# Kernel optimization log

Hardware: AMD Instinct MI355X
Metric: run time of the kernel (lower is better)

Reference implementation:

```python
import jax, jax.numpy as jnp
import numpy as np

CODE_DIMS = [256, 512, 1024, 2048]
C = 256
BETA = 0.25
B = 64
N = 1024


def setup_inputs() -> dict:
    key = jax.random.key(0)
    ks = jax.random.split(key, 2 + len(CODE_DIMS))
    z_e = jax.random.normal(ks[0], (B, N, C), dtype=jnp.float32)
    expert_idx = jax.random.randint(ks[1], (B,), 0, len(CODE_DIMS))
    s = 1.0 / np.sqrt(C)  # torch uniform init bound
    inp = {"z_e": z_e, "expert_idx": expert_idx}
    for r, K in enumerate(CODE_DIMS):
        inp[f"cb{r}"] = jax.random.uniform(ks[2 + r], (K, C), minval=-s, maxval=s, dtype=jnp.float32)
    return inp


def _vq_expert(z_e, cb):
    # z_e: [B, N, C], cb: [K, C]
    Bz, Nz, Cz = z_e.shape
    zf = z_e.reshape(-1, Cz)                                  # [B*N, C]
    dists = ((zf ** 2).sum(axis=1, keepdims=True)
             + (cb ** 2).sum(axis=1)[None, :]
             - 2.0 * zf @ cb.T)                               # [B*N, K]
    idx = jnp.argmin(dists, axis=1)                           # [B*N]
    z_q = cb[idx].reshape(Bz, Nz, Cz)                         # [B, N, C]
    return z_q, idx.reshape(Bz, Nz)


def reference(z_e, expert_idx, cb0, cb1, cb2, cb3):
    cbs = [cb0, cb1, cb2, cb3]
    Bz, Nz, Cz = z_e.shape
    sg = jax.lax.stop_gradient
    z_q_out = jnp.zeros_like(z_e)
    indices = jnp.zeros((Bz, Nz), dtype=jnp.int32)
    vq_loss = jnp.asarray(0.0, dtype=z_e.dtype)
    for r, cb in enumerate(cbs):
        z_q, idx = _vq_expert(z_e, cb)
        mask = expert_idx == r                                # [B]
        mf = mask.astype(z_e.dtype)[:, None, None]            # [B,1,1]
        cnt = mask.sum().astype(z_e.dtype)
        denom = jnp.maximum(cnt * Nz * Cz, 1.0)               # mean over masked subset
        codebook_loss = jnp.sum(mf * (sg(z_q) - z_e) ** 2) / denom
        commit_loss = jnp.sum(mf * (z_q - sg(z_e)) ** 2) / denom
        loss_r = (codebook_loss + BETA * commit_loss) / Cz
        frac = cnt / Bz                                       # z_in.numel()/z_e.numel()
        vq_loss = vq_loss + frac * loss_r
        z_q_st = z_e + sg(z_q - z_e)                          # straight-through
        z_q_out = jnp.where(mf > 0, z_q_st, z_q_out)
        indices = jnp.where(mask[:, None], idx.astype(jnp.int32), indices)
    return z_q_out, indices, vq_loss
```

## Files before the change

kernel.cpp:

```cpp
#include <hip/hip_runtime.h>
#include <hip/hip_bf16.h>


#define EPS_GAP 2e-3f
#define NTOK 65536

typedef __attribute__((ext_vector_type(8))) short bf16x8;
typedef __attribute__((ext_vector_type(4))) float f32x4;

__device__ inline unsigned short f2bf(float f) {
  __hip_bfloat16 h = __float2bfloat16(f);
  unsigned short u;
  __builtin_memcpy(&u, &h, 2);
  return u;
}
__device__ inline float bf2f(unsigned short u) {
  return __uint_as_float(((unsigned)u) << 16);
}

__device__ inline void gll16(const unsigned short* g, unsigned short* l) {
  __builtin_amdgcn_global_load_lds(
      (const __attribute__((address_space(1))) unsigned int*)g,
      (__attribute__((address_space(3))) unsigned int*)l, 16, 0, 0);
}

__global__ __launch_bounds__(256) void csum_split_kernel(
    const float* __restrict__ cb0, const float* __restrict__ cb1,
    const float* __restrict__ cb2, const float* __restrict__ cb3,
    float* __restrict__ csums, double* __restrict__ csums64,
    unsigned short* __restrict__ cb_hi, unsigned short* __restrict__ cb_lo,
    int* __restrict__ wl_cnt) {
  if (blockIdx.x == 0 && threadIdx.x == 0) wl_cnt[0] = 0;
  int row = blockIdx.x * 4 + (threadIdx.x >> 6);
  int lane = threadIdx.x & 63;
  const float* src; int r;
  if (row < 256)       { src = cb0; r = row; }
  else if (row < 768)  { src = cb1; r = row - 256; }
  else if (row < 1792) { src = cb2; r = row - 768; }
  else                 { src = cb3; r = row - 1792; }
  float4 v = ((const float4*)(src + r * 256))[lane];
  unsigned short h0 = f2bf(v.x), h1 = f2bf(v.y), h2 = f2bf(v.z), h3 = f2bf(v.w);
  unsigned short l0 = f2bf(v.x - bf2f(h0)), l1 = f2bf(v.y - bf2f(h1));
  unsigned short l2 = f2bf(v.z - bf2f(h2)), l3 = f2bf(v.w - bf2f(h3));
  *(ushort4*)(cb_hi + (size_t)row * 256 + lane * 4) = make_ushort4(h0, h1, h2, h3);
  *(ushort4*)(cb_lo + (size_t)row * 256 + lane * 4) = make_ushort4(l0, l1, l2, l3);
  double s = (double)v.x*v.x + (double)v.y*v.y + (double)v.z*v.z + (double)v.w*v.w;
  #pragma unroll
  for (int off = 32; off >= 1; off >>= 1) s += __shfl_down(s, off, 64);
  if (lane == 0) { csums[row] = (float)s; csums64[row] = s; }
}

__global__ __launch_bounds__(256) void zsq_kernel(const float* __restrict__ z,
                                                  double* __restrict__ parts) {
  const float4* p = (const float4*)z;
  const int n4 = 4194304;
  double s = 0.0;
  for (int i = blockIdx.x * 256 + threadIdx.x; i < n4; i += 256 * 1024) {
    float4 v = p[i];
    s += (double)v.x*(double)v.x + (double)v.y*(double)v.y
       + (double)v.z*(double)v.z + (double)v.w*(double)v.w;
  }
  #pragma unroll
  for (int off = 32; off >= 1; off >>= 1) s += __shfl_down(s, off, 64);
  __shared__ double sh[4];
  if ((threadIdx.x & 63) == 0) sh[threadIdx.x >> 6] = s;
  __syncthreads();
  if (threadIdx.x == 0) parts[blockIdx.x] = sh[0] + sh[1] + sh[2] + sh[3];
}

__global__ __launch_bounds__(512, 8) void vq_mfma(
    const float* __restrict__ z_e, const int* __restrict__ expert_idx,
    const unsigned short* __restrict__ cb_hi, const unsigned short* __restrict__ cb_lo,
    const float* __restrict__ csums,
    float* __restrict__ D1, int* __restrict__ K1, float* __restrict__ D2) {
  const int b  = blockIdx.y;
  const int e  = expert_idx[b];
  const int hc = blockIdx.z;
  if (hc >= (2 << e)) return;
  const int cs_off = (e == 0) ? 0 : (e == 1) ? 256 : (e == 2) ? 768 : 1792;
  const int krow0  = cs_off + hc * 128;
  const int t0     = b * 1024 + blockIdx.x * 128;

  __shared__ unsigned short smem[4 * 128 * 32];
  __shared__ float  sh_cs[128];
  unsigned short* Ah = smem;
  unsigned short* Al = smem + 128 * 32;
  unsigned short* Bh = smem + 2 * 128 * 32;
  unsigned short* Bl = smem + 3 * 128 * 32;

  const int tid = threadIdx.x;
  if (tid < 128) sh_cs[tid] = csums[krow0 + tid];

  const int w = tid >> 6, l = tid & 63;
  const int h = w >> 2, q = w & 3;
  const int m16 = l & 15, g = l >> 4;

  const int brow   = w * 16 + (l >> 2);
  const int bchunk = (l & 3) ^ ((brow >> 1) & 3);
  const size_t bsrc0 = (size_t)(krow0 + brow) * 256 + (size_t)bchunk * 8;
  unsigned short* bh_dst = Bh + w * 512;
  unsigned short* bl_dst = Bl + w * 512;

  f32x4 acc[4][2];
  #pragma unroll
  for (int i = 0; i < 4; ++i)
    #pragma unroll
    for (int j = 0; j < 2; ++j) acc[i][j] = (f32x4){0.f, 0.f, 0.f, 0.f};

  for (int kp = 0; kp < 8; ++kp) {
    const int kc = kp * 32;
    __syncthreads();
    gll16(cb_hi + bsrc0 + kc, bh_dst);
    gll16(cb_lo + bsrc0 + kc, bl_dst);
    #pragma unroll
    for (int it = 0; it < 2; ++it) {
      int idx = tid + it * 512;
      int row = idx >> 3, seg = idx & 7;
      float4 v = *(const float4*)(z_e + (size_t)(t0 + row) * 256 + kc + seg * 4);
      unsigned hxy, hzw, lxy, lzw;
      asm("v_cvt_pk_bf16_f32 %0, %1, %2" : "=v"(hxy) : "v"(v.x), "v"(v.y));
      asm("v_cvt_pk_bf16_f32 %0, %1, %2" : "=v"(hzw) : "v"(v.z), "v"(v.w));
      float lx = v.x - __uint_as_float(hxy << 16);
      float ly = v.y - __uint_as_float(hxy & 0xffff0000u);
      float lz = v.z - __uint_as_float(hzw << 16);
      float lw = v.w - __uint_as_float(hzw & 0xffff0000u);
      asm("v_cvt_pk_bf16_f32 %0, %1, %2" : "=v"(lxy) : "v"(lx), "v"(ly));
      asm("v_cvt_pk_bf16_f32 %0, %1, %2" : "=v"(lzw) : "v"(lz), "v"(lw));
      int off = row * 32 + ((((seg >> 1) ^ ((row >> 1) & 3)) << 3) | ((seg & 1) << 2));
      *(uint2*)(Ah + off) = make_uint2(hxy, hzw);
      *(uint2*)(Al + off) = make_uint2(lxy, lzw);
    }
    __syncthreads();
    bf16x8 bh[2], bl[2];
    #pragma unroll
    for (int j = 0; j < 2; ++j) {
      int r = q * 32 + j * 16 + m16;
      int n = r * 32 + ((g ^ ((r >> 1) & 3)) << 3);
      bh[j] = *(bf16x8*)(Bh + n);
      bl[j] = *(bf16x8*)(Bl + n);
    }
    #pragma unroll
    for (int i = 0; i < 4; ++i) {
      int r = h * 64 + i * 16 + m16;
      int a = r * 32 + ((g ^ ((r >> 1) & 3)) << 3);
      bf16x8 ah = *(bf16x8*)(Ah + a);
      bf16x8 al = *(bf16x8*)(Al + a);
      #pragma unroll
      for (int j = 0; j < 2; ++j) {
        acc[i][j] = __builtin_amdgcn_mfma_f32_16x16x32_bf16(ah, bh[j], acc[i][j], 0, 0, 0);
        acc[i][j] = __builtin_amdgcn_mfma_f32_16x16x32_bf16(al, bh[j], acc[i][j], 0, 0, 0);
        acc[i][j] = __builtin_amdgcn_mfma_f32_16x16x32_bf16(ah, bl[j], acc[i][j], 0, 0, 0);
      }
    }
  }

  __syncthreads();
  float* mD = (float*)smem;
  int*   mK = (int*)(smem + 1024);
  float* mS = (float*)(smem + 2048);

  #pragma unroll
  for (int i = 0; i < 4; ++i) {
    #pragma unroll
    for (int r = 0; r < 4; ++r) {
      int k0 = q * 32 + m16;
      float d0 = sh_cs[k0]      - 2.0f * acc[i][0][r];
      float d1 = sh_cs[k0 + 16] - 2.0f * acc[i][1][r];
      float bv, sv; int bk;
      if (d0 <= d1) { bv = d0; bk = k0; sv = d1; }
      else          { bv = d1; bk = k0 + 16; sv = d0; }
      #pragma unroll
      for (int off = 8; off >= 1; off >>= 1) {
        float ov = __shfl_xor(bv, off);
        int   ok = __shfl_xor(bk, off);
        float os = __shfl_xor(sv, off);
        float nb; int nk;
        if (ov < bv || (ov == bv && ok < bk)) { nb = ov; nk = ok; }
        else                                  { nb = bv; nk = bk; }
        sv = fminf(fmaxf(bv, ov), fminf(sv, os));
        bv = nb; bk = nk;
      }
      if (m16 == 0) {
        int tloc = h * 64 + i * 16 + g * 4 + r;
        mD[tloc * 4 + q] = bv;
        mK[tloc * 4 + q] = bk;
        mS[tloc * 4 + q] = sv;
      }
    }
  }
  __syncthreads();
  if (tid < 128) {
    float B = 3.4e38f, S = 3.4e38f; int Kb = 0;
    #pragma unroll
    for (int c = 0; c < 4; ++c) {
      float d1v = mD[tid * 4 + c];
      int   k1v = mK[tid * 4 + c];
      float d2v = mS[tid * 4 + c];
      S = fminf(fmaxf(B, d1v), fminf(S, d2v));
      if (d1v < B) { B = d1v; Kb = k1v; }
    }
    int tg = t0 + tid;
    D1[hc * NTOK + tg] = B;
    K1[hc * NTOK + tg] = hc * 128 + Kb;
    D2[hc * NTOK + tg] = S;
  }
}

__global__ __launch_bounds__(256) void combine_kernel(
    const int* __restrict__ expert_idx,
    const float* __restrict__ D1, const int* __restrict__ K1,
    const float* __restrict__ D2,
    float* __restrict__ idx_out,
    int* __restrict__ wl, int* __restrict__ wl_cnt,
    double* __restrict__ parts) {
  const int t = blockIdx.x * 256 + threadIdx.x;
  const int e = expert_idx[t >> 10];
  const int nch = 2 << e;
  float B = 3.4e38f, S = 3.4e38f; int Kb = 0;
  for (int c = 0; c < nch; ++c) {
    float d1 = D1[c * NTOK + t];
    int   k1 = K1[c * NTOK + t];
    float d2 = D2[c * NTOK + t];
    S = fminf(fmaxf(B, d1), fminf(S, d2));
    if (d1 < B) { B = d1; Kb = k1; }
  }
  idx_out[t] = (float)Kb;
  if (S - B < EPS_GAP) {
    int p = atomicAdd(wl_cnt, 1);
    wl[p] = t;
  }
  double s = (double)B;
  #pragma unroll
  for (int off = 32; off >= 1; off >>= 1) s += __shfl_down(s, off, 64);
  __shared__ double sh[4];
  if ((threadIdx.x & 63) == 0) sh[threadIdx.x >> 6] = s;
  __syncthreads();
  if (threadIdx.x == 0) parts[blockIdx.x] = sh[0] + sh[1] + sh[2] + sh[3];
}

__global__ __launch_bounds__(256) void zq_gather_kernel(
    const int* __restrict__ expert_idx,
    const float* __restrict__ cb0, const float* __restrict__ cb1,
    const float* __restrict__ cb2, const float* __restrict__ cb3,
    const float* __restrict__ idx_out, float* __restrict__ zq_out) {
  const int tok  = blockIdx.x * 4 + (threadIdx.x >> 6);
  const int lane = threadIdx.x & 63;
  const int e = expert_idx[tok >> 10];
  const float* cb = (e == 0) ? cb0 : (e == 1) ? cb1 : (e == 2) ? cb2 : cb3;
  const int row = (int)idx_out[tok];
  ((float4*)(zq_out + (size_t)tok * 256))[lane] =
      ((const float4*)(cb + (size_t)row * 256))[lane];
}

__global__ __launch_bounds__(256) void rescue_kernel(
    const float* __restrict__ z_e, const int* __restrict__ expert_idx,
    const float* __restrict__ cb0, const float* __restrict__ cb1,
    const float* __restrict__ cb2, const float* __restrict__ cb3,
    const double* __restrict__ csums64,
    const int* __restrict__ wl, const int* __restrict__ wl_cnt,
    float* __restrict__ zq_out, float* __restrict__ idx_out) {
  __shared__ float  szrow[256];
  __shared__ double szs[4];
  __shared__ float  sdv[3][256];
  __shared__ int    skv[3][256];
  __shared__ int    s_kc;
  const int tid = threadIdx.x;
  const int wid = tid >> 6, lane = tid & 63;
  const int n = wl_cnt[0];
  for (int it = blockIdx.x; it < n; it += gridDim.x) {
    const int t = wl[it];
    const int b = t >> 10;
    const int e = expert_idx[b];
    const int K = 256 << e;
    const float* cb = (e == 0) ? cb0 : (e == 1) ? cb1 : (e == 2) ? cb2 : cb3;
    const int off = (e == 0) ? 0 : (e == 1) ? 256 : (e == 2) ? 768 : 1792;
    const double* cs64 = csums64 + off;

    __syncthreads();
    float zv = z_e[(size_t)t * 256 + tid];
    szrow[tid] = zv;
    double zsq = (double)zv * (double)zv;
    #pragma unroll
    for (int o = 32; o >= 1; o >>= 1) zsq += __shfl_down(zsq, o, 64);
    if (lane == 0) szs[wid] = zsq;
    __syncthreads();
    const float zs_mid = (float)(szs[0] + szs[1] + szs[2] + szs[3]);
    const unsigned zu = __float_as_uint(zs_mid);
    float zs[3] = {__uint_as_float(zu - 1), zs_mid, __uint_as_float(zu + 1)};

    float bd[3] = {3.4e38f, 3.4e38f, 3.4e38f};
    int   bk[3] = {1 << 30, 1 << 30, 1 << 30};
    const float4* z4 = (const float4*)szrow;
    for (int k = tid; k < K; k += 256) {
      const float4* c4 = (const float4*)(cb + (size_t)k * 256);
      double d0 = 0.0, d1v = 0.0, d2v = 0.0, d3 = 0.0;
      for (int qq = 0; qq < 64; qq += 4) {
        float4 a0 = z4[qq],     c0 = c4[qq];
        float4 a1 = z4[qq + 1], c1 = c4[qq + 1];
        float4 a2 = z4[qq + 2], c2 = c4[qq + 2];
        float4 a3 = z4[qq + 3], c3 = c4[qq + 3];
        d0 += (double)a0.x*c0.x + (double)a0.y*c0.y + (double)a0.z*c0.z + (double)a0.w*c0.w;
        d1v+= (double)a1.x*c1.x + (double)a1.y*c1.y + (double)a1.z*c1.z + (double)a1.w*c1.w;
        d2v+= (double)a2.x*c2.x + (double)a2.y*c2.y + (double)a2.z*c2.z + (double)a2.w*c2.w;
        d3 += (double)a3.x*c3.x + (double)a3.y*c3.y + (double)a3.z*c3.z + (double)a3.w*c3.w;
      }
      double dot = (d0 + d1v) + (d2v + d3);
      const float c32 = (float)cs64[k];
      const float m2d = (float)(2.0 * dot);
      #pragma unroll
      for (int v = 0; v < 3; ++v) {
        float T1  = zs[v] + c32;
        float d32 = T1 - m2d;
        if (d32 < bd[v]) { bd[v] = d32; bk[v] = k; }
      }
    }
    #pragma unroll
    for (int v = 0; v < 3; ++v) { sdv[v][tid] = bd[v]; skv[v][tid] = bk[v]; }
    __syncthreads();
    for (int s = 128; s >= 1; s >>= 1) {
      if (tid < s) {
        #pragma unroll
        for (int v = 0; v < 3; ++v) {
          float od = sdv[v][tid + s]; int ok = skv[v][tid + s];
          if (od < sdv[v][tid] || (od == sdv[v][tid] && ok < skv[v][tid])) {
            sdv[v][tid] = od; skv[v][tid] = ok;
          }
        }
      }
      __syncthreads();
    }
    if (tid == 0) {
      int k0 = skv[0][0], k1 = skv[1][0], k2 = skv[2][0];
      int kc = (k0 == k2) ? k0 : k1;
      s_kc = kc;
      idx_out[t] = (float)kc;
    }
    __syncthreads();
    const int kc = s_kc;
    if (tid < 64)
      ((float4*)(zq_out + (size_t)t * 256))[tid] =
          ((const float4*)(cb + (size_t)kc * 256))[tid];
  }
}

__global__ __launch_bounds__(256) void finalize_kernel(
    const double* __restrict__ parts_comb, const double* __restrict__ parts_zsq,
    float* __restrict__ loss_out) {
  const int tid = threadIdx.x;
  double s = parts_comb[tid] + parts_zsq[tid] + parts_zsq[tid + 256]
           + parts_zsq[tid + 512] + parts_zsq[tid + 768];
  #pragma unroll
  for (int off = 32; off >= 1; off >>= 1) s += __shfl_down(s, off, 64);
  __shared__ double sh[4];
  if ((tid & 63) == 0) sh[tid >> 6] = s;
  __syncthreads();
  if (tid == 0)
    loss_out[0] = (float)((sh[0] + sh[1] + sh[2] + sh[3]) * (1.25 / 4294967296.0));
}

extern "C" void kernel_launch(void* const* d_in, const int* in_sizes, int n_in,
                              void* d_out, int out_size, void* d_ws, size_t ws_size,
                              hipStream_t stream) {
  const float* z_e  = (const float*)d_in[0];
  const int*   eidx = (const int*)d_in[1];
  const float* cb0  = (const float*)d_in[2];
  const float* cb1  = (const float*)d_in[3];
  const float* cb2  = (const float*)d_in[4];
  const float* cb3  = (const float*)d_in[5];

  float* zq    = (float*)d_out;
  float* idxf  = (float*)d_out + 16777216;
  float* lossf = (float*)d_out + 16777216 + 65536;

  char* wsp = (char*)d_ws;
  double*         parts_comb = (double*)wsp;           wsp += 256 * 8;
  double*         parts_zsq  = (double*)wsp;           wsp += 1024 * 8;
  double*         csums64    = (double*)wsp;           wsp += 3840 * 8;
  float*          csums      = (float*)wsp;            wsp += 3840 * 4;
  int*            wl_cnt     = (int*)wsp;              wsp += 16;
  int*            wl         = (int*)wsp;              wsp += NTOK * 4;
  unsigned short* cb_hi      = (unsigned short*)wsp;   wsp += 3840 * 256 * 2;
  unsigned short* cb_lo      = (unsigned short*)wsp;   wsp += 3840 * 256 * 2;
  float*          D1         = (float*)wsp;            wsp += 16 * NTOK * 4;
  int*            K1         = (int*)wsp;              wsp += 16 * NTOK * 4;
  float*          D2         = (float*)wsp;            wsp += 16 * NTOK * 4;

  csum_split_kernel<<<960, 256, 0, stream>>>(cb0, cb1, cb2, cb3,
                                             csums, csums64, cb_hi, cb_lo, wl_cnt);
  zsq_kernel<<<1024, 256, 0, stream>>>(z_e, parts_zsq);
  dim3 grid(8, 64, 16);
  vq_mfma<<<grid, 512, 0, stream>>>(z_e, eidx, cb_hi, cb_lo, csums, D1, K1, D2);
  combine_kernel<<<256, 256, 0, stream>>>(eidx, D1, K1, D2, idxf, wl, wl_cnt, parts_comb);
  zq_gather_kernel<<<16384, 256, 0, stream>>>(eidx, cb0, cb1, cb2, cb3, idxf, zq);
  rescue_kernel<<<2048, 256, 0, stream>>>(z_e, eidx, cb0, cb1, cb2, cb3,
                                          csums64, wl, wl_cnt, zq, idxf);
  finalize_kernel<<<1, 256, 0, stream>>>(parts_comb, parts_zsq, lossf);
}
```

Baseline: 425.7 us.

## Double-buffer codebook tiles and register-prefetch z_e in VQ MFMA kernel

Restructures the K-loop of the VQ distance kernel into a software pipeline. The codebook tiles get two LDS buffers, and the next z_e chunk is prefetched into registers while the current one is converted and computed, with explicit waitcnt and barriers. This is meant to hide global-load latency behind MFMA work. In exchange it uses more LDS and registers, so launch_bounds drops from 8 to 4 blocks per SM, which may lower occupancy. Correctness now depends on the hand-written vmcnt counting.

```diff
diff --git a/kernel.cpp b/kernel.cpp
--- a/kernel.cpp
+++ b/kernel.cpp
@@ -68,7 +68,7 @@
   if (threadIdx.x == 0) parts[blockIdx.x] = sh[0] + sh[1] + sh[2] + sh[3];
 }
 
-__global__ __launch_bounds__(512, 8) void vq_mfma(
+__global__ __launch_bounds__(512, 4) void vq_mfma(
     const float* __restrict__ z_e, const int* __restrict__ expert_idx,
     const unsigned short* __restrict__ cb_hi, const unsigned short* __restrict__ cb_lo,
     const float* __restrict__ csums,
@@ -81,12 +81,11 @@
   const int krow0  = cs_off + hc * 128;
   const int t0     = b * 1024 + blockIdx.x * 128;
 
-  __shared__ unsigned short smem[4 * 128 * 32];
+  __shared__ unsigned short smem[6 * 128 * 32];
   __shared__ float  sh_cs[128];
   unsigned short* Ah = smem;
-  unsigned short* Al = smem + 128 * 32;
-  unsigned short* Bh = smem + 2 * 128 * 32;
-  unsigned short* Bl = smem + 3 * 128 * 32;
+  unsigned short* Al = smem + 4096;
+  unsigned short* Bbase = smem + 8192;
 
   const int tid = threadIdx.x;
   if (tid < 128) sh_cs[tid] = csums[krow0 + tid];
@@ -95,11 +94,13 @@
   const int h = w >> 2, q = w & 3;
   const int m16 = l & 15, g = l >> 4;
 
+  const int r0 = tid >> 3, sA = tid & 7;
+  const size_t abase0 = (size_t)(t0 + r0) * 256 + sA * 4;
+  const size_t abase1 = (size_t)(t0 + r0 + 64) * 256 + sA * 4;
+
   const int brow   = w * 16 + (l >> 2);
   const int bchunk = (l & 3) ^ ((brow >> 1) & 3);
   const size_t bsrc0 = (size_t)(krow0 + brow) * 256 + (size_t)bchunk * 8;
-  unsigned short* bh_dst = Bh + w * 512;
-  unsigned short* bl_dst = Bl + w * 512;
 
   f32x4 acc[4][2];
   #pragma unroll
@@ -107,30 +108,63 @@
     #pragma unroll
     for (int j = 0; j < 2; ++j) acc[i][j] = (f32x4){0.f, 0.f, 0.f, 0.f};
 
+  float4 pa0 = *(const float4*)(z_e + abase0);
+  float4 pa1 = *(const float4*)(z_e + abase1);
+  gll16(cb_hi + bsrc0, Bbase + w * 512);
+  gll16(cb_lo + bsrc0, Bbase + 4096 + w * 512);
+
   for (int kp = 0; kp < 8; ++kp) {
-    const int kc = kp * 32;
-    __syncthreads();
-    gll16(cb_hi + bsrc0 + kc, bh_dst);
-    gll16(cb_lo + bsrc0 + kc, bl_dst);
-    #pragma unroll
-    for (int it = 0; it < 2; ++it) {
-      int idx = tid + it * 512;
-      int row = idx >> 3, seg = idx & 7;
-      float4 v = *(const float4*)(z_e + (size_t)(t0 + row) * 256 + kc + seg * 4);
+    const int sel = kp & 1;
+    unsigned short* Bh = Bbase + sel * 8192;
+    unsigned short* Bl = Bh + 4096;
+
+    asm volatile("s_waitcnt lgkmcnt(0)" ::: "memory");
+    __builtin_amdgcn_s_barrier();
+
+    {
       unsigned hxy, hzw, lxy, lzw;
-      asm("v_cvt_pk_bf16_f32 %0, %1, %2" : "=v"(hxy) : "v"(v.x), "v"(v.y));
-      asm("v_cvt_pk_bf16_f32 %0, %1, %2" : "=v"(hzw) : "v"(v.z), "v"(v.w));
-      float lx = v.x - __uint_as_float(hxy << 16);
-      float ly = v.y - __uint_as_float(hxy & 0xffff0000u);
-      float lz = v.z - __uint_as_float(hzw << 16);
-      float lw = v.w - __uint_as_float(hzw & 0xffff0000u);
+      asm("v_cvt_pk_bf16_f32 %0, %1, %2" : "=v"(hxy) : "v"(pa0.x), "v"(pa0.y));
+      asm("v_cvt_pk_bf16_f32 %0, %1, %2" : "=v"(hzw) : "v"(pa0.z), "v"(pa0.w));
+      float lx = pa0.x - __uint_as_float(hxy << 16);
+      float ly = pa0.y - __uint_as_float(hxy & 0xffff0000u);
+      float lz = pa0.z - __uint_as_float(hzw << 16);
+      float lw = pa0.w - __uint_as_float(hzw & 0xffff0000u);
       asm("v_cvt_pk_bf16_f32 %0, %1, %2" : "=v"(lxy) : "v"(lx), "v"(ly));
       asm("v_cvt_pk_bf16_f32 %0, %1, %2" : "=v"(lzw) : "v"(lz), "v"(lw));
-      int off = row * 32 + ((((seg >> 1) ^ ((row >> 1) & 3)) << 3) | ((seg & 1) << 2));
+      int off = r0 * 32 + ((((sA >> 1) ^ ((r0 >> 1) & 3)) << 3) | ((sA & 1) << 2));
       *(uint2*)(Ah + off) = make_uint2(hxy, hzw);
       *(uint2*)(Al + off) = make_uint2(lxy, lzw);
     }
-    __syncthreads();
+    {
+      const int r1 = r0 + 64;
+      unsigned hxy, hzw, lxy, lzw;
+      asm("v_cvt_pk_bf16_f32 %0, %1, %2" : "=v"(hxy) : "v"(pa1.x), "v"(pa1.y));
+      asm("v_cvt_pk_bf16_f32 %0, %1, %2" : "=v"(hzw) : "v"(pa1.z), "v"(pa1.w));
+      float lx = pa1.x - __uint_as_float(hxy << 16);
+      float ly = pa1.y - __uint_as_float(hxy & 0xffff0000u);
+      float lz = pa1.z - __uint_as_float(hzw << 16);
+      float lw = pa1.w - __uint_as_float(hzw & 0xffff0000u);
+      asm("v_cvt_pk_bf16_f32 %0, %1, %2" : "=v"(lxy) : "v"(lx), "v"(ly));
+      asm("v_cvt_pk_bf16_f32 %0, %1, %2" : "=v"(lzw) : "v"(lz), "v"(lw));
+      int off = r1 * 32 + ((((sA >> 1) ^ ((r1 >> 1) & 3)) << 3) | ((sA & 1) << 2));
+      *(uint2*)(Ah + off) = make_uint2(hxy, hzw);
+      *(uint2*)(Al + off) = make_uint2(lxy, lzw);
+    }
+
+    if (kp < 7) {
+      const int kcn = (kp + 1) * 32;
+      pa0 = *(const float4*)(z_e + abase0 + kcn);
+      pa1 = *(const float4*)(z_e + abase1 + kcn);
+      unsigned short* BhN = Bbase + (sel ^ 1) * 8192;
+      gll16(cb_hi + bsrc0 + kcn, BhN + w * 512);
+      gll16(cb_lo + bsrc0 + kcn, BhN + 4096 + w * 512);
+      asm volatile("s_waitcnt vmcnt(4) lgkmcnt(0)" ::: "memory");
+    } else {
+      asm volatile("s_waitcnt vmcnt(0) lgkmcnt(0)" ::: "memory");
+    }
+    __builtin_amdgcn_s_barrier();
+    __builtin_amdgcn_sched_barrier(0);
+
     bf16x8 bh[2], bl[2];
     #pragma unroll
     for (int j = 0; j < 2; ++j) {
```

Measured after the change: 396.6 us. 6.9% less time.

## Pre-split z_e to bf16 hi/lo and double-buffer MFMA loads via async LDS

Applied to the files above, without the earlier changes.

The bf16 hi/lo split of z_e moves out of the MFMA kernel into the existing z-squared reduction kernel, which writes the split arrays into the output buffer as scratch. The MFMA kernel then loads both operands with direct global-to-LDS loads into a double-buffered shared tile, prefetching the next K chunk while computing the current one. This removes repeated per-block fp32 conversion (z_e was converted once per codebook chunk) and overlaps memory with MFMA work. In exchange it writes and reads an extra 64 MB of bf16 data, doubles LDS use and lowers the occupancy hint. It also relies on the output buffer being overwritten later by the gather kernel.

```diff
diff --git a/kernel.cpp b/kernel.cpp
--- a/kernel.cpp
+++ b/kernel.cpp
@@ -50,13 +50,27 @@
   if (lane == 0) { csums[row] = (float)s; csums64[row] = s; }
 }
 
-__global__ __launch_bounds__(256) void zsq_kernel(const float* __restrict__ z,
-                                                  double* __restrict__ parts) {
+__global__ __launch_bounds__(256) void ze_split_kernel(
+    const float* __restrict__ z, unsigned short* __restrict__ ze_hi,
+    unsigned short* __restrict__ ze_lo, double* __restrict__ parts) {
   const float4* p = (const float4*)z;
+  uint2* hi = (uint2*)ze_hi;
+  uint2* lo = (uint2*)ze_lo;
   const int n4 = 4194304;
   double s = 0.0;
   for (int i = blockIdx.x * 256 + threadIdx.x; i < n4; i += 256 * 1024) {
     float4 v = p[i];
+    unsigned hxy, hzw, lxy, lzw;
+    asm("v_cvt_pk_bf16_f32 %0, %1, %2" : "=v"(hxy) : "v"(v.x), "v"(v.y));
+    asm("v_cvt_pk_bf16_f32 %0, %1, %2" : "=v"(hzw) : "v"(v.z), "v"(v.w));
+    float lx = v.x - __uint_as_float(hxy << 16);
+    float ly = v.y - __uint_as_float(hxy & 0xffff0000u);
+    float lz = v.z - __uint_as_float(hzw << 16);
+    float lw = v.w - __uint_as_float(hzw & 0xffff0000u);
+    asm("v_cvt_pk_bf16_f32 %0, %1, %2" : "=v"(lxy) : "v"(lx), "v"(ly));
+    asm("v_cvt_pk_bf16_f32 %0, %1, %2" : "=v"(lzw) : "v"(lz), "v"(lw));
+    hi[i] = make_uint2(hxy, hzw);
+    lo[i] = make_uint2(lxy, lzw);
     s += (double)v.x*(double)v.x + (double)v.y*(double)v.y
        + (double)v.z*(double)v.z + (double)v.w*(double)v.w;
   }
@@ -68,8 +82,9 @@
   if (threadIdx.x == 0) parts[blockIdx.x] = sh[0] + sh[1] + sh[2] + sh[3];
 }
 
-__global__ __launch_bounds__(512, 8) void vq_mfma(
-    const float* __restrict__ z_e, const int* __restrict__ expert_idx,
+__global__ __launch_bounds__(512, 4) void vq_mfma(
+    const unsigned short* __restrict__ ze_hi, const unsigned short* __restrict__ ze_lo,
+    const int* __restrict__ expert_idx,
     const unsigned short* __restrict__ cb_hi, const unsigned short* __restrict__ cb_lo,
     const float* __restrict__ csums,
     float* __restrict__ D1, int* __restrict__ K1, float* __restrict__ D2) {
@@ -81,12 +96,8 @@
   const int krow0  = cs_off + hc * 128;
   const int t0     = b * 1024 + blockIdx.x * 128;
 
-  __shared__ unsigned short smem[4 * 128 * 32];
+  __shared__ unsigned short smem[2 * 4 * 128 * 32];
   __shared__ float  sh_cs[128];
-  unsigned short* Ah = smem;
-  unsigned short* Al = smem + 128 * 32;
-  unsigned short* Bh = smem + 2 * 128 * 32;
-  unsigned short* Bl = smem + 3 * 128 * 32;
 
   const int tid = threadIdx.x;
   if (tid < 128) sh_cs[tid] = csums[krow0 + tid];
@@ -95,11 +106,11 @@
   const int h = w >> 2, q = w & 3;
   const int m16 = l & 15, g = l >> 4;
 
-  const int brow   = w * 16 + (l >> 2);
-  const int bchunk = (l & 3) ^ ((brow >> 1) & 3);
-  const size_t bsrc0 = (size_t)(krow0 + brow) * 256 + (size_t)bchunk * 8;
-  unsigned short* bh_dst = Bh + w * 512;
-  unsigned short* bl_dst = Bl + w * 512;
+  const int srow   = w * 16 + (l >> 2);
+  const int schunk = (l & 3) ^ ((srow >> 1) & 3);
+  const size_t asrc = (size_t)(t0 + srow) * 256 + (size_t)schunk * 8;
+  const size_t bsrc = (size_t)(krow0 + srow) * 256 + (size_t)schunk * 8;
+  const int wslot = w * 512;
 
   f32x4 acc[4][2];
   #pragma unroll
@@ -107,30 +118,30 @@
     #pragma unroll
     for (int j = 0; j < 2; ++j) acc[i][j] = (f32x4){0.f, 0.f, 0.f, 0.f};
 
+  gll16(ze_hi + asrc, smem + wslot);
+  gll16(ze_lo + asrc, smem + 4096 + wslot);
+  gll16(cb_hi + bsrc, smem + 8192 + wslot);
+  gll16(cb_lo + bsrc, smem + 12288 + wslot);
+
   for (int kp = 0; kp < 8; ++kp) {
-    const int kc = kp * 32;
-    __syncthreads();
-    gll16(cb_hi + bsrc0 + kc, bh_dst);
-    gll16(cb_lo + bsrc0 + kc, bl_dst);
-    #pragma unroll
-    for (int it = 0; it < 2; ++it) {
-      int idx = tid + it * 512;
-      int row = idx >> 3, seg = idx & 7;
-      float4 v = *(const float4*)(z_e + (size_t)(t0 + row) * 256 + kc + seg * 4);
-      unsigned hxy, hzw, lxy, lzw;
-      asm("v_cvt_pk_bf16_f32 %0, %1, %2" : "=v"(hxy) : "v"(v.x), "v"(v.y));
-      asm("v_cvt_pk_bf16_f32 %0, %1, %2" : "=v"(hzw) : "v"(v.z), "v"(v.w));
-      float lx = v.x - __uint_as_float(hxy << 16);
-      float ly = v.y - __uint_as_float(hxy & 0xffff0000u);
-      float lz = v.z - __uint_as_float(hzw << 16);
-      float lw = v.w - __uint_as_float(hzw & 0xffff0000u);
-      asm("v_cvt_pk_bf16_f32 %0, %1, %2" : "=v"(lxy) : "v"(lx), "v"(ly));
-      asm("v_cvt_pk_bf16_f32 %0, %1, %2" : "=v"(lzw) : "v"(lz), "v"(lw));
-      int off = row * 32 + ((((seg >> 1) ^ ((row >> 1) & 3)) << 3) | ((seg & 1) << 2));
-      *(uint2*)(Ah + off) = make_uint2(hxy, hzw);
-      *(uint2*)(Al + off) = make_uint2(lxy, lzw);
-    }
-    __syncthreads();
+    unsigned short* buf = smem + (kp & 1) * 16384;
+    if (kp < 7) {
+      const int kcn = (kp + 1) * 32;
+      unsigned short* nb = smem + ((kp & 1) ^ 1) * 16384;
+      gll16(ze_hi + asrc + kcn, nb + wslot);
+      gll16(ze_lo + asrc + kcn, nb + 4096 + wslot);
+      gll16(cb_hi + bsrc + kcn, nb + 8192 + wslot);
+      gll16(cb_lo + bsrc + kcn, nb + 12288 + wslot);
+      asm volatile("s_waitcnt vmcnt(4)" ::: "memory");
+    } else {
+      asm volatile("s_waitcnt vmcnt(0)" ::: "memory");
+    }
+    __builtin_amdgcn_s_barrier();
+
+    unsigned short* Ah = buf;
+    unsigned short* Al = buf + 4096;
+    unsigned short* Bh = buf + 8192;
+    unsigned short* Bl = buf + 12288;
     bf16x8 bh[2], bl[2];
     #pragma unroll
     for (int j = 0; j < 2; ++j) {
@@ -152,6 +163,8 @@
         acc[i][j] = __builtin_amdgcn_mfma_f32_16x16x32_bf16(ah, bl[j], acc[i][j], 0, 0, 0);
       }
     }
+    __builtin_amdgcn_sched_barrier(0);
+    __builtin_amdgcn_s_barrier();
   }
 
   __syncthreads();
@@ -372,6 +385,9 @@
   float* idxf  = (float*)d_out + 16777216;
   float* lossf = (float*)d_out + 16777216 + 65536;
 
+  unsigned short* ze_hi = (unsigned short*)d_out;
+  unsigned short* ze_lo = ze_hi + 16777216;
+
   char* wsp = (char*)d_ws;
   double*         parts_comb = (double*)wsp;           wsp += 256 * 8;
   double*         parts_zsq  = (double*)wsp;           wsp += 1024 * 8;
@@ -387,9 +403,9 @@
 
   csum_split_kernel<<<960, 256, 0, stream>>>(cb0, cb1, cb2, cb3,
                                              csums, csums64, cb_hi, cb_lo, wl_cnt);
-  zsq_kernel<<<1024, 256, 0, stream>>>(z_e, parts_zsq);
+  ze_split_kernel<<<1024, 256, 0, stream>>>(z_e, ze_hi, ze_lo, parts_zsq);
   dim3 grid(8, 64, 16);
-  vq_mfma<<<grid, 512, 0, stream>>>(z_e, eidx, cb_hi, cb_lo, csums, D1, K1, D2);
+  vq_mfma<<<grid, 512, 0, stream>>>(ze_hi, ze_lo, eidx, cb_hi, cb_lo, csums, D1, K1, D2);
   combine_kernel<<<256, 256, 0, stream>>>(eidx, D1, K1, D2, idxf, wl, wl_cnt, parts_comb);
   zq_gather_kernel<<<16384, 256, 0, stream>>>(eidx, cb0, cb1, cb2, cb3, idxf, zq);
   rescue_kernel<<<2048, 256, 0, stream>>>(z_e, eidx, cb0, cb1, cb2, cb3,
```

New measurement: 399.5 us. -6.1%, faster.
